# Optimization experiments

Measured on AMD Instinct MI355X. Metric: run time of the kernel, lower is better.

Reference implementation:

```python
import jax, jax.numpy as jnp
import numpy as np

DILATED = (1, 2, 3)
NUM_PROTOS = 100
PROTO_SIZE = 4
ENC_SIZE = 1600
NUM_CLASSES = 2
B, L = 64, 256

# num_filters split exactly as in torch: floor(P/len) each, first gets remainder
_nf = [NUM_PROTOS // len(DILATED)] * len(DILATED)
_nf[0] += NUM_PROTOS % len(DILATED)
NUM_FILTERS = tuple(_nf)  # (34, 33, 33)


def setup_inputs() -> dict:
    key = jax.random.key(0)
    k1, k2, k3 = jax.random.split(key, 3)
    embedding = jax.random.normal(k1, (B, L, ENC_SIZE), dtype=jnp.float32)
    # nn.init.uniform_ default is U[0,1)
    protolayer = jax.random.uniform(k2, (NUM_PROTOS, ENC_SIZE, PROTO_SIZE), dtype=jnp.float32)
    fc_w = jax.random.normal(k3, (NUM_CLASSES, NUM_PROTOS), dtype=jnp.float32) * 0.1
    return {"embedding": embedding, "protolayer": protolayer, "fc_w": fc_w}


def _l2_convolution(x_bel, protolayer):
    # x_bel: [B, L, E] -> [B, E, L] for NCH conv layout
    x = jnp.transpose(x_bel, (0, 2, 1))
    # sliding-window sum of x^2 computed ONCE per dilation (shared across protos,
    # mathematically identical to conv1d with all-ones weight)
    s = jnp.sum(x * x, axis=1)  # [B, L]
    p2_sum = jnp.sum(protolayer * protolayer, axis=(1, 2))  # [P]
    distances = []
    j = 0
    Lx = x.shape[2]
    for d, n in zip(DILATED, NUM_FILTERS):
        L_out = Lx - (PROTO_SIZE - 1) * d
        # windowed sum over K=PROTO_SIZE taps with dilation d: [B, L_out]
        x2_patch = sum(s[:, k * d:k * d + L_out] for k in range(PROTO_SIZE))
        # dilated cross-correlation x * p : [B, n, L_out]
        xp = jax.lax.conv_general_dilated(
            x, protolayer[j:j + n],
            window_strides=(1,), padding='VALID', rhs_dilation=(d,),
            dimension_numbers=('NCH', 'OIH', 'NCH'))
        dist = jnp.sqrt(jnp.abs(x2_patch[:, None, :] - 2.0 * xp
                                + p2_sum[j:j + n][None, :, None]))
        distances.append(dist)
        j += n
    return distances


def reference(embedding, protolayer, fc_w):
    distances = _l2_convolution(embedding, protolayer)
    prototype_distances = jnp.concatenate(
        [jnp.min(d, axis=2) for d in distances], axis=1)  # [B, P]
    class_out = prototype_distances @ fc_w.T  # [B, num_classes]
    return (prototype_distances, distances[0], distances[1], distances[2], class_out)
```

## Files before the change

### kernel.cpp

```cpp
#include <hip/hip_runtime.h>

#define B_   64
#define L_   256
#define E_   1600
#define P_   100
#define KP   4
#define N0 34
#define N1 33
#define N2 33
#define LOUT0 253
#define LOUT1 250
#define LOUT2 247
#define OFF_PD 0
#define OFF_D0 6400
#define OFF_D1 (OFF_D0 + B_*N0*LOUT0)
#define OFF_D2 (OFF_D1 + B_*N1*LOUT1)
#define OFF_CO (OFF_D2 + B_*N2*LOUT2)

#define WS_ABF  0ull
#define WS_BT   52428800ull
#define WS_S    (WS_BT + 1280000ull)
#define WS_P2   (WS_S + 65536ull)
#define WS_CNT  (WS_P2 + 512ull)
#define WS_NEED (WS_CNT + 256ull)

#define TMF  96
#define BKB  128
#define BOFF2 12288
#define BUFSZ 22528

typedef float f32x4 __attribute__((ext_vector_type(4)));
typedef unsigned short ushort8v __attribute__((ext_vector_type(8)));
typedef __bf16 bf16x8 __attribute__((ext_vector_type(8)));
typedef _Float16 f16;

__device__ __forceinline__ unsigned short bf16rne(float f) {
    unsigned u = __float_as_uint(f);
    u += 0x7FFFu + ((u >> 16) & 1u);
    return (unsigned short)(u >> 16);
}

typedef __attribute__((address_space(3))) void lds_void_t;
typedef __attribute__((address_space(1))) void glb_void_t;

__device__ __forceinline__ void gload16(const void* g, void* l) {
    __builtin_amdgcn_global_load_lds((const glb_void_t*)g, (lds_void_t*)l, 16, 0, 0);
}


__global__ __launch_bounds__(256) void proto_prep_fast(
        const float* __restrict__ emb, const float* __restrict__ proto,
        char* __restrict__ ws, float* __restrict__ out) {
    int q = blockIdx.x;
    int wave = threadIdx.x >> 6, lane = threadIdx.x & 63;
    if (q < 4096) {
        int row = q * 4 + wave;
        const float4* r = (const float4*)(emb + (size_t)row * E_);
        unsigned short* dst = (unsigned short*)(ws + WS_ABF + (size_t)row * (E_*2));
        float acc = 0.f;
        #pragma unroll
        for (int it = 0; it < 6; ++it) {
            int e4 = it * 64 + lane;
            float4 v = r[e4];
            acc += v.x*v.x + v.y*v.y + v.z*v.z + v.w*v.w;
            ushort4 bv = make_ushort4(bf16rne(v.x), bf16rne(v.y),
                                      bf16rne(v.z), bf16rne(v.w));
            *(ushort4*)(dst + e4 * 4) = bv;
        }
        if (lane < 16) {
            int e4 = 384 + lane;
            float4 v = r[e4];
            acc += v.x*v.x + v.y*v.y + v.z*v.z + v.w*v.w;
            ushort4 bv = make_ushort4(bf16rne(v.x), bf16rne(v.y),
                                      bf16rne(v.z), bf16rne(v.w));
            *(ushort4*)(dst + e4 * 4) = bv;
        }
        #pragma unroll
        for (int off = 32; off; off >>= 1) acc += __shfl_down(acc, off);
        if (lane == 0) ((float*)(ws + WS_S))[row] = acc;
    } else if (q < 4121) {
        int p = (q - 4096) * 4 + wave;
        if (p < P_) {
            const float4* r = (const float4*)(proto + (size_t)p * (E_ * KP));
            unsigned short* bt = (unsigned short*)(ws + WS_BT);
            float acc = 0.f;
            #pragma unroll
            for (int it = 0; it < 25; ++it) {
                int e = it * 64 + lane;
                float4 v = r[e];
                acc += v.x*v.x + v.y*v.y + v.z*v.z + v.w*v.w;
                bt[(size_t)(4*p + 0) * E_ + e] = bf16rne(v.x);
                bt[(size_t)(4*p + 1) * E_ + e] = bf16rne(v.y);
                bt[(size_t)(4*p + 2) * E_ + e] = bf16rne(v.z);
                bt[(size_t)(4*p + 3) * E_ + e] = bf16rne(v.w);
            }
            #pragma unroll
            for (int off = 32; off; off >>= 1) acc += __shfl_down(acc, off);
            if (lane == 0) ((float*)(ws + WS_P2))[p] = acc;
        }
    } else {
        for (int i = threadIdx.x; i < B_ * P_; i += 256)
            out[OFF_PD + i] = __uint_as_float(0x7F800000u);
        if (threadIdx.x < 64)
            ((unsigned*)(ws + WS_CNT))[threadIdx.x] = 0u;
    }
}

__global__ __launch_bounds__(384, 4) void proto_main_fast(
        char* __restrict__ ws, const float* __restrict__ fc_w,
        float* __restrict__ out) {

    __shared__ __align__(16) char smem[2 * BUFSZ];
    __shared__ int lastf;

    int bx   = blockIdx.x;
    int lb   = (bx & 7) * 120 + (bx >> 3);
    int b     = lb / 15;
    int inner = lb % 15;
    int m     = inner / 5;
    int n_blk = inner % 5;
    int r0    = (m == 0) ? 0 : (m == 1 ? 87 : 160);
    int l_lo  = m * 87;
    int pbase = n_blk * 20;

    const char* Ag = ws + WS_ABF + (size_t)(b * L_ + r0) * (E_ * 2);
    const char* Bg = ws + WS_BT  + (size_t)(pbase * 4) * (E_ * 2);

    int tid   = threadIdx.x;
    int lane  = tid & 63;
    int wave  = tid >> 6;
    int mrow  = lane & 15;
    int jq    = lane >> 4;
    int lrow8 = lane >> 3;
    int jst   = lane & 7;

    f32x4 acc[5] = {};

    for (int t = wave; t < 22; t += 6) {
        if (t < 12) {
            int rowl = t * 8 + lrow8;
            int j = jst ^ (rowl & 7);
            gload16(Ag + (size_t)rowl * (E_*2) + j * 16, smem + t * 1024);
        } else {
            int rowl = (t - 12) * 8 + lrow8;
            int j = jst ^ (rowl & 7);
            gload16(Bg + (size_t)rowl * (E_*2) + j * 16,
                    smem + BOFF2 + (t - 12) * 1024);
        }
    }
    __syncthreads();

    for (int c = 0; c < 25; ++c) {
        const char* cbuf = smem + (c & 1) * BUFSZ;
        if (c < 24) {
            char* nbuf = smem + ((c + 1) & 1) * BUFSZ;
            int eoff = (c + 1) * BKB;
            for (int t = wave; t < 22; t += 6) {
                if (t < 12) {
                    int rowl = t * 8 + lrow8;
                    int j = jst ^ (rowl & 7);
                    gload16(Ag + (size_t)rowl * (E_*2) + eoff + j * 16,
                            nbuf + t * 1024);
                } else {
                    int rowl = (t - 12) * 8 + lrow8;
                    int j = jst ^ (rowl & 7);
                    gload16(Bg + (size_t)rowl * (E_*2) + eoff + j * 16,
                            nbuf + BOFF2 + (t - 12) * 1024);
                }
            }
        }
        #pragma unroll
        for (int ks = 0; ks < 2; ++ks) {
            int rowA = wave * 16 + mrow;
            ushort8v af = *(const ushort8v*)(cbuf + rowA * 128
                            + (((ks << 2) + jq) ^ (rowA & 7)) * 16);
            ushort8v bfv[5];
            #pragma unroll
            for (int ni = 0; ni < 5; ++ni) {
                int rowB = ni * 16 + mrow;
                bfv[ni] = *(const ushort8v*)(cbuf + BOFF2 + rowB * 128
                            + (((ks << 2) + jq) ^ (rowB & 7)) * 16);
            }
            #pragma unroll
            for (int ni = 0; ni < 5; ++ni)
                acc[ni] = __builtin_amdgcn_mfma_f32_16x16x32_bf16(
                    __builtin_bit_cast(bf16x8, af),
                    __builtin_bit_cast(bf16x8, bfv[ni]),
                    acc[ni], 0, 0, 0);
        }
        __syncthreads();
    }

    f16*      Yh     = (f16*)smem;
    float*    slds   = (float*)(smem + 15552);
    float*    p2lds  = slds + TMF;
    unsigned* minlds = (unsigned*)(p2lds + 20);

    {
        int colq = lane & 15;
        int rowq = (lane >> 4) * 4;
        int row = wave * 16 + rowq;
        #pragma unroll
        for (int ni = 0; ni < 5; ++ni) {
            int col = ni * 16 + colq;
            #pragma unroll
            for (int r = 0; r < 4; ++r)
                Yh[(row + r) * 81 + col] = (f16)acc[ni][r];
        }
    }
    if (tid < TMF) slds[tid] = ((const float*)(ws + WS_S))[b * L_ + r0 + tid];
    if (tid < 20) {
        p2lds[tid] = ((const float*)(ws + WS_P2))[pbase + tid];
        minlds[tid] = 0x7F800000u;
    }
    __syncthreads();

    for (int idx = tid; idx < 20 * 87; idx += 384) {
        int pl  = idx / 87;
        int lof = idx % 87;
        int p = pbase + pl;
        int d, Lout, nseg, pseg; size_t segbase;
        if (p < 34)      { d = 1; Lout = LOUT0; segbase = OFF_D0; pseg = p;      nseg = N0; }
        else if (p < 67) { d = 2; Lout = LOUT1; segbase = OFF_D1; pseg = p - 34; nseg = N1; }
        else             { d = 3; Lout = LOUT2; segbase = OFF_D2; pseg = p - 67; nseg = N2; }
        int l = l_lo + lof;
        if (l < Lout) {
            int rl = l - r0;
            int c0 = pl * 4;
            float xp = (float)Yh[rl * 81 + c0]
                     + (float)Yh[(rl + d) * 81 + c0 + 1]
                     + (float)Yh[(rl + 2*d) * 81 + c0 + 2]
                     + (float)Yh[(rl + 3*d) * 81 + c0 + 3];
            float x2 = slds[rl] + slds[rl + d] + slds[rl + 2*d] + slds[rl + 3*d];
            float dist = sqrtf(fabsf(x2 - 2.f * xp + p2lds[pl]));
            out[segbase + ((size_t)b * nseg + pseg) * Lout + l] = dist;
            atomicMin(&minlds[pl], __float_as_uint(dist));
        }
    }
    __syncthreads();
    if (tid < 20)
        atomicMin((unsigned*)out + OFF_PD + b * P_ + pbase + tid, minlds[tid]);

    __syncthreads();
    if (tid == 0) {
        __threadfence();
        unsigned prev = atomicAdd((unsigned*)(ws + WS_CNT) + b, 1u);
        lastf = (prev == 14u);
    }
    __syncthreads();
    if (lastf && tid < 128) {
        int cls = tid >> 6;
        int ln  = tid & 63;
        float s = 0.f;
        for (int p = ln; p < P_; p += 64) {
            float v = __hip_atomic_load(
                (const float*)out + OFF_PD + b * P_ + p,
                __ATOMIC_RELAXED, __HIP_MEMORY_SCOPE_AGENT);
            s += v * fc_w[cls * P_ + p];
        }
        #pragma unroll
        for (int off = 32; off; off >>= 1) s += __shfl_down(s, off);
        if (ln == 0) out[OFF_CO + b * 2 + cls] = s;
    }
}

#define TM   144
#define ASTR 40
#define YSTR 81

__global__ __launch_bounds__(256) void proto_prep_kernel(
        const float* __restrict__ emb, const float* __restrict__ proto,
        float* __restrict__ ws_s, float* __restrict__ ws_p2,
        float* __restrict__ out) {
    int q = blockIdx.x;
    int wave = threadIdx.x >> 6, lane = threadIdx.x & 63;
    if (q < 4096) {
        int row = q * 4 + wave;
        const float4* r = (const float4*)(emb + (size_t)row * E_);
        float acc = 0.f;
        #pragma unroll
        for (int it = 0; it < 7; ++it) {
            int e4 = it * 64 + lane;
            if (e4 < 400) {
                float4 v = r[e4];
                acc += v.x*v.x + v.y*v.y + v.z*v.z + v.w*v.w;
            }
        }
        #pragma unroll
        for (int off = 32; off; off >>= 1) acc += __shfl_down(acc, off);
        if (lane == 0) ws_s[row] = acc;
    } else if (q < 4121) {
        int p = (q - 4096) * 4 + wave;
        if (p < P_) {
            const float4* r = (const float4*)(proto + (size_t)p * (E_ * KP));
            float acc = 0.f;
            #pragma unroll
            for (int it = 0; it < 25; ++it) {
                float4 v = r[it * 64 + lane];
                acc += v.x*v.x + v.y*v.y + v.z*v.z + v.w*v.w;
            }
            #pragma unroll
            for (int off = 32; off; off >>= 1) acc += __shfl_down(acc, off);
            if (lane == 0) ws_p2[p] = acc;
        }
    } else {
        for (int i = threadIdx.x; i < B_ * P_; i += 256)
            out[OFF_PD + i] = __uint_as_float(0x7F800000u);
    }
}

__global__ __launch_bounds__(192) void proto_main_kernel(
        const float* __restrict__ emb, const float* __restrict__ proto,
        const float* __restrict__ ws_s, const float* __restrict__ ws_p2,
        float* __restrict__ out) {

    __shared__ __align__(16) char smem[47392];
    unsigned short* Ald = (unsigned short*)smem;
    unsigned short* Bld = (unsigned short*)(smem + TM*ASTR*2);

    int bx = blockIdx.x;
    int n_blk = bx % 5;
    int m     = (bx / 5) & 1;
    int b     = bx / 10;
    int r0    = m ? 112 : 0;
    int pbase = n_blk * 20;

    const float* Abase = emb + ((size_t)(b * L_ + r0)) * E_;
    const float* Bbase = proto + (size_t)pbase * (E_ * KP);

    int tid  = threadIdx.x;
    int lane = tid & 63;
    int wave = tid >> 6;
    int mrow = lane & 15;
    int kq   = (lane >> 4) * 8;

    f32x4 acc[3][5] = {};

    for (int c = 0; c < E_ / 32; ++c) {
        int e0 = c * 32;
        #pragma unroll
        for (int i = 0; i < 6; ++i) {
            int idx = tid + i * 192;
            int row = idx >> 3;
            int e4  = idx & 7;
            float4 v = *(const float4*)(Abase + (size_t)row * E_ + e0 + e4 * 4);
            ushort4 bv = make_ushort4(bf16rne(v.x), bf16rne(v.y),
                                      bf16rne(v.z), bf16rne(v.w));
            *(ushort4*)&Ald[row * ASTR + e4 * 4] = bv;
        }
        for (int idx = tid; idx < 640; idx += 192) {
            int pl = idx >> 5;
            int el = idx & 31;
            float4 v = *(const float4*)(Bbase + (size_t)pl * (E_ * KP)
                                        + (size_t)(e0 + el) * KP);
            Bld[(4*pl + 0) * ASTR + el] = bf16rne(v.x);
            Bld[(4*pl + 1) * ASTR + el] = bf16rne(v.y);
            Bld[(4*pl + 2) * ASTR + el] = bf16rne(v.z);
            Bld[(4*pl + 3) * ASTR + el] = bf16rne(v.w);
        }
        __syncthreads();

        ushort8v af[3], bfr[5];
        #pragma unroll
        for (int mi = 0; mi < 3; ++mi)
            af[mi] = *(const ushort8v*)&Ald[(wave*48 + mi*16 + mrow) * ASTR + kq];
        #pragma unroll
        for (int ni = 0; ni < 5; ++ni)
            bfr[ni] = *(const ushort8v*)&Bld[(ni*16 + mrow) * ASTR + kq];
        #pragma unroll
        for (int mi = 0; mi < 3; ++mi)
            #pragma unroll
            for (int ni = 0; ni < 5; ++ni)
                acc[mi][ni] = __builtin_amdgcn_mfma_f32_16x16x32_bf16(
                    __builtin_bit_cast(bf16x8, af[mi]),
                    __builtin_bit_cast(bf16x8, bfr[ni]),
                    acc[mi][ni], 0, 0, 0);
        __syncthreads();
    }

    float*    Ylds   = (float*)smem;
    float*    slds   = (float*)(smem + TM * YSTR * 4);
    float*    p2lds  = slds + TM;
    unsigned* minlds = (unsigned*)(p2lds + 20);

    {
        int colq = lane & 15;
        int rowq = (lane >> 4) * 4;
        #pragma unroll
        for (int mi = 0; mi < 3; ++mi) {
            int row = wave * 48 + mi * 16 + rowq;
            #pragma unroll
            for (int ni = 0; ni < 5; ++ni) {
                int col = ni * 16 + colq;
                #pragma unroll
                for (int r = 0; r < 4; ++r)
                    Ylds[(row + r) * YSTR + col] = acc[mi][ni][r];
            }
        }
    }
    if (tid < TM) slds[tid] = ws_s[b * L_ + r0 + tid];
    if (tid < 20) { p2lds[tid] = ws_p2[pbase + tid]; minlds[tid] = 0x7F800000u; }
    __syncthreads();

    int l_lo = m * 128;
    for (int idx = tid; idx < 20 * 128; idx += 192) {
        int pl  = idx >> 7;
        int lof = idx & 127;
        int p = pbase + pl;
        int d, Lout, nseg, pseg; size_t segbase;
        if (p < 34)      { d = 1; Lout = LOUT0; segbase = OFF_D0; pseg = p;      nseg = N0; }
        else if (p < 67) { d = 2; Lout = LOUT1; segbase = OFF_D1; pseg = p - 34; nseg = N1; }
        else             { d = 3; Lout = LOUT2; segbase = OFF_D2; pseg = p - 67; nseg = N2; }
        int l = l_lo + lof;
        if (l < Lout) {
            int rl = l - r0;
            int c0 = pl * 4;
            float xp = Ylds[rl * YSTR + c0]
                     + Ylds[(rl + d) * YSTR + c0 + 1]
                     + Ylds[(rl + 2*d) * YSTR + c0 + 2]
                     + Ylds[(rl + 3*d) * YSTR + c0 + 3];
            float x2 = slds[rl] + slds[rl + d] + slds[rl + 2*d] + slds[rl + 3*d];
            float dist = sqrtf(fabsf(x2 - 2.f * xp + p2lds[pl]));
            out[segbase + ((size_t)b * nseg + pseg) * Lout + l] = dist;
            atomicMin(&minlds[pl], __float_as_uint(dist));
        }
    }
    __syncthreads();
    if (tid < 20)
        atomicMin((unsigned*)out + OFF_PD + b * P_ + pbase + tid, minlds[tid]);
}

__global__ __launch_bounds__(128) void proto_fc_kernel(
        const float* __restrict__ fc_w, float* __restrict__ out) {
    int t = threadIdx.x;
    int b = t >> 1, c = t & 1;
    const float* pd = out + OFF_PD + b * P_;
    const float* w  = fc_w + c * P_;
    float s = 0.f;
    #pragma unroll 4
    for (int p = 0; p < P_; ++p) s += pd[p] * w[p];
    out[OFF_CO + b * 2 + c] = s;
}

extern "C" void kernel_launch(void* const* d_in, const int* in_sizes, int n_in,
                              void* d_out, int out_size, void* d_ws, size_t ws_size,
                              hipStream_t stream) {
    const float* emb   = (const float*)d_in[0];
    const float* proto = (const float*)d_in[1];
    const float* fc_w  = (const float*)d_in[2];
    float* out  = (float*)d_out;

    if (ws_size >= WS_NEED) {
        char* ws = (char*)d_ws;
        proto_prep_fast<<<4122, 256, 0, stream>>>(emb, proto, ws, out);
        proto_main_fast<<<960, 384, 0, stream>>>(ws, fc_w, out);
    } else {
        float* ws_s  = (float*)d_ws;
        float* ws_p2 = ws_s + B_ * L_;
        proto_prep_kernel<<<4122, 256, 0, stream>>>(emb, proto, ws_s, ws_p2, out);
        proto_main_kernel<<<640, 192, 0, stream>>>(emb, proto, ws_s, ws_p2, out);
        proto_fc_kernel<<<1, 128, 0, stream>>>(fc_w, out);
    }
}
```

Baseline: 240.2 us.

## Triple-buffer GEMM K-loop with finer chunks and vmcnt-based waits

The main MFMA loop moves from a double-buffered scheme with 128-byte K chunks and full __syncthreads to a triple-buffered ring of 64-byte chunks (50 phases). Each wave issues exactly two async global->LDS loads per phase and synchronises with explicit s_waitcnt vmcnt and s_barrier, so two loads stay in flight. It also raises MFMA priority with s_setprio and raises the occupancy hint to 6 blocks per CU, since LDS per block shrinks to 36 KB. The cost is more barriers per unit of work, and the higher occupancy hint may force register spills.

```diff
diff --git a/kernel.cpp b/kernel.cpp
--- a/kernel.cpp
+++ b/kernel.cpp
@@ -24,10 +24,9 @@
 #define WS_CNT  (WS_P2 + 512ull)
 #define WS_NEED (WS_CNT + 256ull)
 
-#define TMF  96
-#define BKB  128
-#define BOFF2 12288
-#define BUFSZ 22528
+#define TMF   96
+#define BUF1  12288
+#define NPH   50
 
 typedef float f32x4 __attribute__((ext_vector_type(4)));
 typedef unsigned short ushort8v __attribute__((ext_vector_type(8)));
@@ -46,6 +45,11 @@
 __device__ __forceinline__ void gload16(const void* g, void* l) {
     __builtin_amdgcn_global_load_lds((const glb_void_t*)g, (lds_void_t*)l, 16, 0, 0);
 }
+
+#define VWAIT4() asm volatile("s_waitcnt vmcnt(4)" ::: "memory")
+#define VWAIT2() asm volatile("s_waitcnt vmcnt(2)" ::: "memory")
+#define VWAIT0() asm volatile("s_waitcnt vmcnt(0)" ::: "memory")
+#define SBAR()   asm volatile("s_barrier" ::: "memory")
 
 
 __global__ __launch_bounds__(256) void proto_prep_fast(
@@ -106,11 +110,11 @@
     }
 }
 
-__global__ __launch_bounds__(384, 4) void proto_main_fast(
+__global__ __launch_bounds__(384, 6) void proto_main_fast(
         char* __restrict__ ws, const float* __restrict__ fc_w,
         float* __restrict__ out) {
 
-    __shared__ __align__(16) char smem[2 * BUFSZ];
+    __shared__ __align__(64) char smem[3 * BUF1];
     __shared__ int lastf;
 
     int bx   = blockIdx.x;
@@ -131,65 +135,66 @@
     int wave  = tid >> 6;
     int mrow  = lane & 15;
     int jq    = lane >> 4;
-    int lrow8 = lane >> 3;
-    int jst   = lane & 7;
+
+    int t0 = wave * 2, t1 = t0 + 1;
+    int r_in = lane >> 2;
+    int j16  = (((lane & 3) ^ (r_in & 3)) << 4);
+    const char* q0 = (t0 < 6 ? Ag + (size_t)(t0 * 16 + r_in) * (E_*2)
+                             : Bg + (size_t)((t0 - 6) * 16 + r_in) * (E_*2)) + j16;
+    const char* q1 = (t1 < 6 ? Ag + (size_t)(t1 * 16 + r_in) * (E_*2)
+                             : Bg + (size_t)((t1 - 6) * 16 + r_in) * (E_*2)) + j16;
+    int l0 = t0 * 1024, l1 = t1 * 1024;
+
+    int sx     = ((jq ^ (mrow & 3)) << 4);
+    int aoff   = (wave * 16 + mrow) * 64 + sx;
+    int boff   = 6144 + mrow * 64 + sx;
 
     f32x4 acc[5] = {};
 
-    for (int t = wave; t < 22; t += 6) {
-        if (t < 12) {
-            int rowl = t * 8 + lrow8;
-            int j = jst ^ (rowl & 7);
-            gload16(Ag + (size_t)rowl * (E_*2) + j * 16, smem + t * 1024);
-        } else {
-            int rowl = (t - 12) * 8 + lrow8;
-            int j = jst ^ (rowl & 7);
-            gload16(Bg + (size_t)rowl * (E_*2) + j * 16,
-                    smem + BOFF2 + (t - 12) * 1024);
-        }
-    }
-    __syncthreads();
-
-    for (int c = 0; c < 25; ++c) {
-        const char* cbuf = smem + (c & 1) * BUFSZ;
-        if (c < 24) {
-            char* nbuf = smem + ((c + 1) & 1) * BUFSZ;
-            int eoff = (c + 1) * BKB;
-            for (int t = wave; t < 22; t += 6) {
-                if (t < 12) {
-                    int rowl = t * 8 + lrow8;
-                    int j = jst ^ (rowl & 7);
-                    gload16(Ag + (size_t)rowl * (E_*2) + eoff + j * 16,
-                            nbuf + t * 1024);
-                } else {
-                    int rowl = (t - 12) * 8 + lrow8;
-                    int j = jst ^ (rowl & 7);
-                    gload16(Bg + (size_t)rowl * (E_*2) + eoff + j * 16,
-                            nbuf + BOFF2 + (t - 12) * 1024);
-                }
-            }
-        }
-        #pragma unroll
-        for (int ks = 0; ks < 2; ++ks) {
-            int rowA = wave * 16 + mrow;
-            ushort8v af = *(const ushort8v*)(cbuf + rowA * 128
-                            + (((ks << 2) + jq) ^ (rowA & 7)) * 16);
-            ushort8v bfv[5];
-            #pragma unroll
-            for (int ni = 0; ni < 5; ++ni) {
-                int rowB = ni * 16 + mrow;
-                bfv[ni] = *(const ushort8v*)(cbuf + BOFF2 + rowB * 128
-                            + (((ks << 2) + jq) ^ (rowB & 7)) * 16);
-            }
-            #pragma unroll
-            for (int ni = 0; ni < 5; ++ni)
-                acc[ni] = __builtin_amdgcn_mfma_f32_16x16x32_bf16(
-                    __builtin_bit_cast(bf16x8, af),
-                    __builtin_bit_cast(bf16x8, bfv[ni]),
-                    acc[ni], 0, 0, 0);
-        }
-        __syncthreads();
-    }
+    #pragma unroll
+    for (int k = 0; k < 3; ++k) {
+        gload16(q0, smem + k * BUF1 + l0);
+        gload16(q1, smem + k * BUF1 + l1);
+        q0 += 64; q1 += 64;
+    }
+
+    char* cb = smem;
+    int curi = 0;
+
+    #define COMPUTE_PHASE(CBUF)                                              \
+    {                                                                        \
+        ushort8v af = *(const ushort8v*)((CBUF) + aoff);                     \
+        ushort8v bfv[5];                                                     \
+        _Pragma("unroll")                                                    \
+        for (int ni = 0; ni < 5; ++ni)                                       \
+            bfv[ni] = *(const ushort8v*)((CBUF) + boff + ni * 1024);         \
+        __builtin_amdgcn_s_setprio(1);                                       \
+        _Pragma("unroll")                                                    \
+        for (int ni = 0; ni < 5; ++ni)                                       \
+            acc[ni] = __builtin_amdgcn_mfma_f32_16x16x32_bf16(               \
+                __builtin_bit_cast(bf16x8, af),                              \
+                __builtin_bit_cast(bf16x8, bfv[ni]),                         \
+                acc[ni], 0, 0, 0);                                           \
+        __builtin_amdgcn_s_setprio(0);                                       \
+    }
+
+    for (int c = 0; c < 47; ++c) {
+        VWAIT4();
+        SBAR();
+        COMPUTE_PHASE(cb);
+        SBAR();
+        gload16(q0, cb + l0);
+        gload16(q1, cb + l1);
+        q0 += 64; q1 += 64;
+        cb += BUF1; if (++curi == 3) { curi = 0; cb = smem; }
+    }
+    VWAIT4(); SBAR(); COMPUTE_PHASE(cb);
+    cb += BUF1; if (++curi == 3) { curi = 0; cb = smem; }
+    VWAIT2(); SBAR(); COMPUTE_PHASE(cb);
+    cb += BUF1; if (++curi == 3) { curi = 0; cb = smem; }
+    VWAIT0(); SBAR(); COMPUTE_PHASE(cb);
+
+    __syncthreads();
 
     f16*      Yh     = (f16*)smem;
     float*    slds   = (float*)(smem + 15552);
@@ -262,6 +267,7 @@
         for (int off = 32; off; off >>= 1) s += __shfl_down(s, off);
         if (ln == 0) out[OFF_CO + b * 2 + cls] = s;
     }
+    #undef COMPUTE_PHASE
 }
 
 #define TM   144
```

Result: slower. 257.5 us (+7.2%).

## Enlarge M tile to 144 rows with register-resident A fragments

Applied to the files above, without the earlier changes.

Each block now covers 144 sequence rows (two row-blocks per batch instead of three), using 3 waves that each own 48 rows. A operands are loaded straight from global memory into registers and prefetched one step ahead, while only the B tile goes through double-buffered LDS. MFMA sections are wrapped in s_setprio. The aim is fewer redundant halo loads and more MFMAs per LDS read, which cuts the A-traffic through LDS. The cost is fewer blocks (640), fewer waves per block, and more registers per thread.

```diff
diff --git a/kernel.cpp b/kernel.cpp
--- a/kernel.cpp
+++ b/kernel.cpp
@@ -24,10 +24,9 @@
 #define WS_CNT  (WS_P2 + 512ull)
 #define WS_NEED (WS_CNT + 256ull)
 
-#define TMF  96
-#define BKB  128
-#define BOFF2 12288
-#define BUFSZ 22528
+#define TMW   144
+#define BBUF  10240
+#define AROWB 51200
 
 typedef float f32x4 __attribute__((ext_vector_type(4)));
 typedef unsigned short ushort8v __attribute__((ext_vector_type(8)));
@@ -106,118 +105,138 @@
     }
 }
 
-__global__ __launch_bounds__(384, 4) void proto_main_fast(
+__global__ __launch_bounds__(192, 3) void proto_main_fast(
         char* __restrict__ ws, const float* __restrict__ fc_w,
         float* __restrict__ out) {
 
-    __shared__ __align__(16) char smem[2 * BUFSZ];
+    __shared__ __align__(64) char smem[24576];
     __shared__ int lastf;
 
-    int bx   = blockIdx.x;
-    int lb   = (bx & 7) * 120 + (bx >> 3);
-    int b     = lb / 15;
-    int inner = lb % 15;
+    int bx = blockIdx.x;
+    int lb = (bx & 7) * 80 + (bx >> 3);
+    int b     = lb / 10;
+    int inner = lb % 10;
     int m     = inner / 5;
     int n_blk = inner % 5;
-    int r0    = (m == 0) ? 0 : (m == 1 ? 87 : 160);
-    int l_lo  = m * 87;
+    int r0    = m ? 112 : 0;
     int pbase = n_blk * 20;
 
     const char* Ag = ws + WS_ABF + (size_t)(b * L_ + r0) * (E_ * 2);
     const char* Bg = ws + WS_BT  + (size_t)(pbase * 4) * (E_ * 2);
 
-    int tid   = threadIdx.x;
-    int lane  = tid & 63;
-    int wave  = tid >> 6;
-    int mrow  = lane & 15;
-    int jq    = lane >> 4;
-    int lrow8 = lane >> 3;
-    int jst   = lane & 7;
-
-    f32x4 acc[5] = {};
-
-    for (int t = wave; t < 22; t += 6) {
-        if (t < 12) {
-            int rowl = t * 8 + lrow8;
-            int j = jst ^ (rowl & 7);
-            gload16(Ag + (size_t)rowl * (E_*2) + j * 16, smem + t * 1024);
-        } else {
-            int rowl = (t - 12) * 8 + lrow8;
-            int j = jst ^ (rowl & 7);
-            gload16(Bg + (size_t)rowl * (E_*2) + j * 16,
-                    smem + BOFF2 + (t - 12) * 1024);
-        }
-    }
+    int tid  = threadIdx.x;
+    int lane = tid & 63;
+    int wave = tid >> 6;
+    int mrow = lane & 15;
+    int jq   = lane >> 4;
+
+    int srow  = lane >> 3;
+    int sslot = lane & 7;
+
+    const char* Aw = Ag + (size_t)(wave * 48 + mrow) * (E_*2) + jq * 16;
+
+    f32x4 acc[3][5] = {};
+    ushort8v a_cur[3][2], a_nxt[3][2];
+
+    #pragma unroll
+    for (int t0 = 0; t0 < 4; ++t0) {
+        int t = wave + t0 * 3;
+        if (t < 10) {
+            int row = t * 8 + srow;
+            gload16(Bg + (size_t)row * (E_*2) + ((sslot ^ (row & 7)) << 4),
+                    smem + t * 1024);
+        }
+    }
+    #pragma unroll
+    for (int mi = 0; mi < 3; ++mi)
+        #pragma unroll
+        for (int ks = 0; ks < 2; ++ks)
+            a_cur[mi][ks] = *(const ushort8v*)(Aw + mi * AROWB + ks * 64);
     __syncthreads();
 
     for (int c = 0; c < 25; ++c) {
-        const char* cbuf = smem + (c & 1) * BUFSZ;
+        const char* cbuf = smem + (c & 1) * BBUF;
+        char* nbuf = (char*)smem + ((c + 1) & 1) * BBUF;
         if (c < 24) {
-            char* nbuf = smem + ((c + 1) & 1) * BUFSZ;
-            int eoff = (c + 1) * BKB;
-            for (int t = wave; t < 22; t += 6) {
-                if (t < 12) {
-                    int rowl = t * 8 + lrow8;
-                    int j = jst ^ (rowl & 7);
-                    gload16(Ag + (size_t)rowl * (E_*2) + eoff + j * 16,
+            int eoff = (c + 1) * 128;
+            #pragma unroll
+            for (int t0 = 0; t0 < 4; ++t0) {
+                int t = wave + t0 * 3;
+                if (t < 10) {
+                    int row = t * 8 + srow;
+                    gload16(Bg + (size_t)row * (E_*2) + eoff
+                              + ((sslot ^ (row & 7)) << 4),
                             nbuf + t * 1024);
-                } else {
-                    int rowl = (t - 12) * 8 + lrow8;
-                    int j = jst ^ (rowl & 7);
-                    gload16(Bg + (size_t)rowl * (E_*2) + eoff + j * 16,
-                            nbuf + BOFF2 + (t - 12) * 1024);
                 }
             }
+            #pragma unroll
+            for (int mi = 0; mi < 3; ++mi)
+                #pragma unroll
+                for (int ks = 0; ks < 2; ++ks)
+                    a_nxt[mi][ks] = *(const ushort8v*)(Aw + eoff
+                                        + mi * AROWB + ks * 64);
         }
         #pragma unroll
         for (int ks = 0; ks < 2; ++ks) {
-            int rowA = wave * 16 + mrow;
-            ushort8v af = *(const ushort8v*)(cbuf + rowA * 128
-                            + (((ks << 2) + jq) ^ (rowA & 7)) * 16);
             ushort8v bfv[5];
             #pragma unroll
             for (int ni = 0; ni < 5; ++ni) {
                 int rowB = ni * 16 + mrow;
-                bfv[ni] = *(const ushort8v*)(cbuf + BOFF2 + rowB * 128
-                            + (((ks << 2) + jq) ^ (rowB & 7)) * 16);
-            }
-            #pragma unroll
-            for (int ni = 0; ni < 5; ++ni)
-                acc[ni] = __builtin_amdgcn_mfma_f32_16x16x32_bf16(
-                    __builtin_bit_cast(bf16x8, af),
-                    __builtin_bit_cast(bf16x8, bfv[ni]),
-                    acc[ni], 0, 0, 0);
+                bfv[ni] = *(const ushort8v*)(cbuf + rowB * 128
+                            + ((((ks << 2) + jq) ^ (rowB & 7)) << 4));
+            }
+            __builtin_amdgcn_s_setprio(1);
+            #pragma unroll
+            for (int mi = 0; mi < 3; ++mi)
+                #pragma unroll
+                for (int ni = 0; ni < 5; ++ni)
+                    acc[mi][ni] = __builtin_amdgcn_mfma_f32_16x16x32_bf16(
+                        __builtin_bit_cast(bf16x8, a_cur[mi][ks]),
+                        __builtin_bit_cast(bf16x8, bfv[ni]),
+                        acc[mi][ni], 0, 0, 0);
+            __builtin_amdgcn_s_setprio(0);
         }
         __syncthreads();
+        if (c < 24) {
+            #pragma unroll
+            for (int mi = 0; mi < 3; ++mi)
+                #pragma unroll
+                for (int ks = 0; ks < 2; ++ks)
+                    a_cur[mi][ks] = a_nxt[mi][ks];
+        }
     }
 
     f16*      Yh     = (f16*)smem;
-    float*    slds   = (float*)(smem + 15552);
-    float*    p2lds  = slds + TMF;
+    float*    slds   = (float*)(smem + 23328);
+    float*    p2lds  = slds + TMW;
     unsigned* minlds = (unsigned*)(p2lds + 20);
 
     {
         int colq = lane & 15;
         int rowq = (lane >> 4) * 4;
-        int row = wave * 16 + rowq;
-        #pragma unroll
-        for (int ni = 0; ni < 5; ++ni) {
-            int col = ni * 16 + colq;
-            #pragma unroll
-            for (int r = 0; r < 4; ++r)
-                Yh[(row + r) * 81 + col] = (f16)acc[ni][r];
-        }
-    }
-    if (tid < TMF) slds[tid] = ((const float*)(ws + WS_S))[b * L_ + r0 + tid];
+        #pragma unroll
+        for (int mi = 0; mi < 3; ++mi) {
+            int row = wave * 48 + mi * 16 + rowq;
+            #pragma unroll
+            for (int ni = 0; ni < 5; ++ni) {
+                int col = ni * 16 + colq;
+                #pragma unroll
+                for (int r = 0; r < 4; ++r)
+                    Yh[(row + r) * 81 + col] = (f16)acc[mi][ni][r];
+            }
+        }
+    }
+    if (tid < TMW) slds[tid] = ((const float*)(ws + WS_S))[b * L_ + r0 + tid];
     if (tid < 20) {
         p2lds[tid] = ((const float*)(ws + WS_P2))[pbase + tid];
         minlds[tid] = 0x7F800000u;
     }
     __syncthreads();
 
-    for (int idx = tid; idx < 20 * 87; idx += 384) {
-        int pl  = idx / 87;
-        int lof = idx % 87;
+    int l_lo = m * 128;
+    for (int idx = tid; idx < 20 * 128; idx += 192) {
+        int pl  = idx >> 7;
+        int lof = idx & 127;
         int p = pbase + pl;
         int d, Lout, nseg, pseg; size_t segbase;
         if (p < 34)      { d = 1; Lout = LOUT0; segbase = OFF_D0; pseg = p;      nseg = N0; }
@@ -245,7 +264,7 @@
     if (tid == 0) {
         __threadfence();
         unsigned prev = atomicAdd((unsigned*)(ws + WS_CNT) + b, 1u);
-        lastf = (prev == 14u);
+        lastf = (prev == 9u);
     }
     __syncthreads();
     if (lastf && tid < 128) {
@@ -453,7 +472,7 @@
     if (ws_size >= WS_NEED) {
         char* ws = (char*)d_ws;
         proto_prep_fast<<<4122, 256, 0, stream>>>(emb, proto, ws, out);
-        proto_main_fast<<<960, 384, 0, stream>>>(ws, fc_w, out);
+        proto_main_fast<<<640, 192, 0, stream>>>(ws, fc_w, out);
     } else {
         float* ws_s  = (float*)d_ws;
         float* ws_p2 = ws_s + B_ * L_;
```

Measured after the change: 236.3 us. About the same (-1.6%).

## Load A fragments directly into registers, stage only B tile through LDS

Applied to the files above, without the earlier changes.

The A operand (embedding rows) is now read straight from global memory into MFMA register fragments, prefetched one chunk ahead, instead of being staged through LDS. Only the B (prototype) tile is double-buffered in shared memory, which shrinks LDS use and removes the LDS write/read traffic for A. The trade-off is that A comes through uncoalesced 16-byte per-lane global loads whose latency must be hidden by the register prefetch, and register pressure rises slightly.

```diff
diff --git a/kernel.cpp b/kernel.cpp
--- a/kernel.cpp
+++ b/kernel.cpp
@@ -24,10 +24,8 @@
 #define WS_CNT  (WS_P2 + 512ull)
 #define WS_NEED (WS_CNT + 256ull)
 
-#define TMF  96
-#define BKB  128
-#define BOFF2 12288
-#define BUFSZ 22528
+#define TMF   96
+#define BBUF  10240
 
 typedef float f32x4 __attribute__((ext_vector_type(4)));
 typedef unsigned short ushort8v __attribute__((ext_vector_type(8)));
@@ -110,7 +108,7 @@
         char* __restrict__ ws, const float* __restrict__ fc_w,
         float* __restrict__ out) {
 
-    __shared__ __align__(16) char smem[2 * BUFSZ];
+    __shared__ __align__(64) char smem[2 * BBUF];
     __shared__ int lastf;
 
     int bx   = blockIdx.x;
@@ -126,69 +124,62 @@
     const char* Ag = ws + WS_ABF + (size_t)(b * L_ + r0) * (E_ * 2);
     const char* Bg = ws + WS_BT  + (size_t)(pbase * 4) * (E_ * 2);
 
-    int tid   = threadIdx.x;
-    int lane  = tid & 63;
-    int wave  = tid >> 6;
-    int mrow  = lane & 15;
-    int jq    = lane >> 4;
-    int lrow8 = lane >> 3;
-    int jst   = lane & 7;
+    int tid  = threadIdx.x;
+    int lane = tid & 63;
+    int wave = tid >> 6;
+    int mrow = lane & 15;
+    int jq   = lane >> 4;
+
+    int srow  = lane >> 3;
+    int sslot = lane & 7;
+    int t0 = wave, t1 = wave + 6;
+    int row0 = t0 * 8 + srow;
+    int row1 = t1 * 8 + srow;
+    const char* Bq0 = Bg + (size_t)row0 * (E_*2) + ((sslot ^ (row0 & 7)) << 4);
+    const char* Bq1 = Bg + (size_t)row1 * (E_*2) + ((sslot ^ (row1 & 7)) << 4);
+
+    const char* Aw = Ag + (size_t)(wave * 16 + mrow) * (E_*2) + jq * 16;
 
     f32x4 acc[5] = {};
-
-    for (int t = wave; t < 22; t += 6) {
-        if (t < 12) {
-            int rowl = t * 8 + lrow8;
-            int j = jst ^ (rowl & 7);
-            gload16(Ag + (size_t)rowl * (E_*2) + j * 16, smem + t * 1024);
-        } else {
-            int rowl = (t - 12) * 8 + lrow8;
-            int j = jst ^ (rowl & 7);
-            gload16(Bg + (size_t)rowl * (E_*2) + j * 16,
-                    smem + BOFF2 + (t - 12) * 1024);
-        }
-    }
+    ushort8v a_cur[2], a_nxt[2];
+
+    gload16(Bq0, smem + t0 * 1024);
+    if (t1 < 10) gload16(Bq1, smem + t1 * 1024);
+    a_cur[0] = *(const ushort8v*)(Aw);
+    a_cur[1] = *(const ushort8v*)(Aw + 64);
     __syncthreads();
 
     for (int c = 0; c < 25; ++c) {
-        const char* cbuf = smem + (c & 1) * BUFSZ;
+        const char* cbuf = smem + (c & 1) * BBUF;
+        char* nbuf = (char*)smem + ((c + 1) & 1) * BBUF;
         if (c < 24) {
-            char* nbuf = smem + ((c + 1) & 1) * BUFSZ;
-            int eoff = (c + 1) * BKB;
-            for (int t = wave; t < 22; t += 6) {
-                if (t < 12) {
-                    int rowl = t * 8 + lrow8;
-                    int j = jst ^ (rowl & 7);
-                    gload16(Ag + (size_t)rowl * (E_*2) + eoff + j * 16,
-                            nbuf + t * 1024);
-                } else {
-                    int rowl = (t - 12) * 8 + lrow8;
-                    int j = jst ^ (rowl & 7);
-                    gload16(Bg + (size_t)rowl * (E_*2) + eoff + j * 16,
-                            nbuf + BOFF2 + (t - 12) * 1024);
-                }
-            }
+            int eoff = (c + 1) * 128;
+            gload16(Bq0 + eoff, nbuf + t0 * 1024);
+            if (t1 < 10) gload16(Bq1 + eoff, nbuf + t1 * 1024);
+            a_nxt[0] = *(const ushort8v*)(Aw + eoff);
+            a_nxt[1] = *(const ushort8v*)(Aw + eoff + 64);
         }
         #pragma unroll
         for (int ks = 0; ks < 2; ++ks) {
-            int rowA = wave * 16 + mrow;
-            ushort8v af = *(const ushort8v*)(cbuf + rowA * 128
-                            + (((ks << 2) + jq) ^ (rowA & 7)) * 16);
             ushort8v bfv[5];
             #pragma unroll
             for (int ni = 0; ni < 5; ++ni) {
                 int rowB = ni * 16 + mrow;
-                bfv[ni] = *(const ushort8v*)(cbuf + BOFF2 + rowB * 128
-                            + (((ks << 2) + jq) ^ (rowB & 7)) * 16);
+                bfv[ni] = *(const ushort8v*)(cbuf + rowB * 128
+                            + ((((ks << 2) + jq) ^ (rowB & 7)) << 4));
             }
             #pragma unroll
             for (int ni = 0; ni < 5; ++ni)
                 acc[ni] = __builtin_amdgcn_mfma_f32_16x16x32_bf16(
-                    __builtin_bit_cast(bf16x8, af),
+                    __builtin_bit_cast(bf16x8, a_cur[ks]),
                     __builtin_bit_cast(bf16x8, bfv[ni]),
                     acc[ni], 0, 0, 0);
         }
         __syncthreads();
+        if (c < 24) {
+            a_cur[0] = a_nxt[0];
+            a_cur[1] = a_nxt[1];
+        }
     }
 
     f16*      Yh     = (f16*)smem;
```

Result: slower. 251.4 us (+4.7%).
